# Kernel tuning notes

Hardware: AMD Instinct MI355X
Metric: run time of the kernel (lower is better)

Reference implementation:

```python
import jax, jax.numpy as jnp
import numpy as np

N = 50000      # nodes
E = 1200000    # edges
G = 256        # graphs in batch
H = 64         # hidden_dim
F_IN = 5       # input_dim
L = 3          # num deep GCN layers
EPS_BN = 1e-5
EPS_MSG = 1e-7

def setup_inputs() -> dict:
    key = jax.random.key(0)
    ks = jax.random.split(key, 12)
    r = lambda i, shp, s=0.1: jax.random.normal(ks[i], shp, jnp.float32) * s
    return {
        "x": jax.random.normal(ks[0], (N, F_IN), jnp.float32),
        "edge_index": jax.random.randint(ks[1], (2, E), 0, N),
        "batch_idx": jnp.sort(jax.random.randint(ks[2], (N,), 0, G)),
        "conv1_W": r(3, (F_IN, H)), "conv1_b": jnp.zeros((H,), jnp.float32),
        "bn1_g": jnp.ones((H,), jnp.float32), "bn1_b": jnp.zeros((H,), jnp.float32),
        "ln_g": jnp.ones((L, H), jnp.float32), "ln_b": jnp.zeros((L, H), jnp.float32),
        "prelu_a": jnp.full((L, H), 0.25, jnp.float32),
        "gen_t": jnp.ones((L,), jnp.float32),
        "mlp_W1": r(4, (L, H, 2 * H)), "mlp_b1": jnp.zeros((L, 2 * H), jnp.float32),
        "mlp_bn_g": jnp.ones((L, 2 * H), jnp.float32), "mlp_bn_b": jnp.zeros((L, 2 * H), jnp.float32),
        "mlp_W2": r(5, (L, 2 * H, H)), "mlp_b2": jnp.zeros((L, H), jnp.float32),
        "lin1_W": r(6, ((L + 1) * H * 2, 2 * H)), "lin1_b": jnp.zeros((2 * H,), jnp.float32),
        "lin2_W": r(7, (2 * H, H)), "lin2_b": jnp.zeros((H,), jnp.float32),
        "out_W": r(8, (H, 1)), "out_b": jnp.zeros((1,), jnp.float32),
    }

def _layernorm(x, g, b):
    mu = jnp.mean(x, axis=-1, keepdims=True)
    var = jnp.mean(jnp.square(x - mu), axis=-1, keepdims=True)
    return (x - mu) * jax.lax.rsqrt(var + EPS_BN) * g + b

def _prelu(x, a):
    return jnp.where(x >= 0, x, a * x)

def _bn_eval(x, g, b):
    # eval-mode BatchNorm with running_mean=0, running_var=1
    return x * (g / jnp.sqrt(1.0 + EPS_BN)) + b

def reference(x, edge_index, batch_idx, conv1_W, conv1_b, bn1_g, bn1_b,
              ln_g, ln_b, prelu_a, gen_t, mlp_W1, mlp_b1, mlp_bn_g, mlp_bn_b,
              mlp_W2, mlp_b2, lin1_W, lin1_b, lin2_W, lin2_b, out_W, out_b):
    n = x.shape[0]
    src, dst = edge_index[0], edge_index[1]

    # ---- GCNConv (with self loops, symmetric normalization) ----
    loops = jnp.arange(n)
    row = jnp.concatenate([src, loops])  # [E+N]
    col = jnp.concatenate([dst, loops])
    h = x @ conv1_W
    deg = jax.ops.segment_sum(jnp.ones_like(col, jnp.float32), col, num_segments=n)
    dinv = jnp.where(deg > 0, deg ** -0.5, 0.0)
    norm = dinv[row] * dinv[col]
    h = jax.ops.segment_sum(h[row] * norm[:, None], col, num_segments=n) + conv1_b
    h = _bn_eval(h, bn1_g, bn1_b)
    h = jax.nn.relu(h)

    xs = [h]
    # ---- DeepGCNLayer (res+) x L, GENConv with softmax aggregation ----
    for i in range(ln_g.shape[0]):
        u = _layernorm(h, ln_g[i], ln_b[i])
        u = _prelu(u, prelu_a[i])
        msg = jax.nn.relu(u[src]) + EPS_MSG            # [E, H]
        sc = msg * gen_t[i]
        m = jax.ops.segment_max(sc, dst, num_segments=n)
        e = jnp.exp(sc - m[dst])
        s = jax.ops.segment_sum(e, dst, num_segments=n)
        alpha = e / s[dst]                             # segment-wise softmax per channel
        agg = jax.ops.segment_sum(msg * alpha, dst, num_segments=n) + u  # root add
        z = agg @ mlp_W1[i] + mlp_b1[i]
        z = _bn_eval(z, mlp_bn_g[i], mlp_bn_b[i])
        z = jax.nn.relu(z)
        z = z @ mlp_W2[i] + mlp_b2[i]
        h = h + z                                      # res+
        xs.append(h)

    # ---- JumpingKnowledge cat + global mean/max pool ----
    xc = jnp.concatenate(xs, axis=1)                   # [N, 4H]
    cnt = jax.ops.segment_sum(jnp.ones((n,), jnp.float32), batch_idx, num_segments=G)
    xmean = jax.ops.segment_sum(xc, batch_idx, num_segments=G) / jnp.maximum(cnt, 1.0)[:, None]
    xmax = jax.ops.segment_max(xc, batch_idx, num_segments=G)
    xmax = jnp.where(jnp.isfinite(xmax), xmax, 0.0)
    p = jnp.concatenate([xmean, xmax], axis=1)         # [G, 8H]

    # ---- readout MLP (dropout off in eval) ----
    p = jax.nn.relu(p @ lin1_W + lin1_b)
    p = jax.nn.relu(p @ lin2_W + lin2_b)
    return p @ out_W + out_b
```

## Files before the change

### kernel.cpp

```cpp
#include <hip/hip_runtime.h>
#include <math.h>

#define NND 50000
#define NE  1200000
#define NG  256
#define H   64
#define H2  128
#define H4  256
#define H8  512
#define FIN 5
#define EPS_BN 1e-5f
#define EPS_MSG 1e-7f
#define NB 196
#define TILES 196
#define TCAP 7168
#define EPB 4096
#define NB1 293
#define ELLC 72
#define PC 8
#define MT 64

typedef _Float16 half8 __attribute__((ext_vector_type(8)));
typedef _Float16 half4 __attribute__((ext_vector_type(4)));
typedef float floatx4 __attribute__((ext_vector_type(4)));


__global__ void k_setup(const int* __restrict__ batch, int* tilecur, int* __restrict__ gstart,
                        const float* __restrict__ x, float* __restrict__ xp,
                        const float* __restrict__ W1, const float* __restrict__ W2,
                        _Float16* __restrict__ w1f, _Float16* __restrict__ w2f) {
    int b = blockIdx.x, t = threadIdx.x;
    if (b < NB) {
        int n = b * 256 + t;
        if (n < NND) {
            float a0 = x[n * FIN + 0], a1 = x[n * FIN + 1], a2 = x[n * FIN + 2];
            float a3 = x[n * FIN + 3], a4 = x[n * FIN + 4];
            *(float4*)&xp[n * 8] = make_float4(a0, a1, a2, a3);
            *(float4*)&xp[n * 8 + 4] = make_float4(a4, 0.f, 0.f, 0.f);
        }
        return;
    }
    if (b == NB || b == NB + 1) {
        if (b == NB && t < TILES) tilecur[t] = 0;
        int g = (b - NB) * 256 + t;
        if (g > NG) return;
        int lo = 0, hi = NND;
        while (lo < hi) { int mid = (lo + hi) >> 1; if (batch[mid] < g) lo = mid + 1; else hi = mid; }
        gstart[g] = lo;
        return;
    }
    int tt = (b - NB - 2) * 256 + t;
    if (tt >= 3 * 16 * 64) return;
    int lane = tt & 63, fr = (tt >> 6) & 15, l = tt >> 10;
    {
        int jt = fr >> 1, kf = fr & 1;
        int j = jt * 16 + (lane & 15);
        int k0 = kf * 32 + (lane >> 4) * 8;
#pragma unroll
        for (int i = 0; i < 8; i++)
            w1f[(((size_t)l * 16 + jt * 2 + kf) * 64 + lane) * 8 + i] =
                (_Float16)W1[(size_t)l * H * H2 + (k0 + i) * H2 + j];
    }
    {
        int ct = fr >> 2, k2f = fr & 3;
        int c = ct * 16 + (lane & 15);
        int k0 = k2f * 32 + (lane >> 4) * 8;
#pragma unroll
        for (int i = 0; i < 8; i++)
            w2f[(((size_t)l * 16 + ct * 4 + k2f) * 64 + lane) * 8 + i] =
                (_Float16)W2[(size_t)l * H2 * H + (k0 + i) * H + c];
    }
}


__global__ void __launch_bounds__(256)
k_bin1(const int* __restrict__ ei, int* tilecur, unsigned* __restrict__ tilebuf) {
    __shared__ int cnt[TILES];
    __shared__ int base[TILES];
    int b = blockIdx.x, t = threadIdx.x;
    for (int i = t; i < TILES; i += 256) cnt[i] = 0;
    __syncthreads();
    int e0 = b * EPB;
#pragma unroll
    for (int r = 0; r < EPB / 256; r++) {
        int e = e0 + r * 256 + t;
        if (e < NE) atomicAdd(&cnt[ei[NE + e] >> 8], 1);
    }
    __syncthreads();
    for (int i = t; i < TILES; i += 256) {
        base[i] = atomicAdd(&tilecur[i], cnt[i]);
        cnt[i] = 0;
    }
    __syncthreads();
#pragma unroll
    for (int r = 0; r < EPB / 256; r++) {
        int e = e0 + r * 256 + t;
        if (e < NE) {
            int s = ei[e], d = ei[NE + e];
            int tile = d >> 8;
            int pos = base[tile] + atomicAdd(&cnt[tile], 1);
            if (pos < TCAP)
                tilebuf[(size_t)tile * TCAP + pos] = ((unsigned)s << 8) | (unsigned)(d & 255);
        }
    }
}

__global__ void __launch_bounds__(256)
k_bin2(const int* __restrict__ tilecur, const unsigned* __restrict__ tilebuf,
       unsigned short* __restrict__ ell, int* __restrict__ deg, float* __restrict__ dinv) {
    __shared__ unsigned short ell_l[256 * ELLC];
    __shared__ int cnt[256];
    int tile = blockIdx.x, t = threadIdx.x;
    cnt[t] = 0;
    __syncthreads();
    int n = min(tilecur[tile], TCAP);
    for (int i = t; i < n; i += 256) {
        unsigned v = tilebuf[(size_t)tile * TCAP + i];
        int dl = v & 255u;
        int slot = atomicAdd(&cnt[dl], 1);
        if (slot < ELLC) ell_l[dl * ELLC + slot] = (unsigned short)(v >> 8);
    }
    __syncthreads();
    const unsigned* s32 = (const unsigned*)ell_l;
    unsigned* d32 = (unsigned*)(ell + (size_t)tile * 256 * ELLC);
    for (int i = t; i < 256 * ELLC / 2; i += 256) d32[i] = s32[i];
    int d = tile * 256 + t;
    if (d < NND) {
        deg[d] = min(cnt[t], ELLC);
        dinv[d] = rsqrtf((float)cnt[t] + 1.0f);
    }
}


__global__ void k_gcn(const int* __restrict__ deg, const unsigned short* __restrict__ ell,
                      const float* __restrict__ xp, const float* __restrict__ dinv,
                      const float* __restrict__ W,
                      const float* __restrict__ cb, const float* __restrict__ bg,
                      const float* __restrict__ bb,
                      const float* __restrict__ lg, const float* __restrict__ lb,
                      const float* __restrict__ pa,
                      float* __restrict__ xc, _Float16* __restrict__ u_h) {
    int d = (blockIdx.x * blockDim.x + threadIdx.x) >> 6;
    int lane = threadIdx.x & 63;
    if (d >= NND) return;
    int dg = deg[d];
    size_t base = (size_t)d * ELLC;
    float xw0 = 0.f, xw1 = 0.f, xw2 = 0.f, xw3 = 0.f, xw4 = 0.f;
    for (int i = lane; i < dg; i += 64) {
        int s = (int)ell[base + i];
        float dv = dinv[s];
        float4 a = *(const float4*)&xp[s * 8];
        float a4 = xp[s * 8 + 4];
        xw0 += a.x * dv; xw1 += a.y * dv; xw2 += a.z * dv;
        xw3 += a.w * dv; xw4 += a4 * dv;
    }
#pragma unroll
    for (int off = 1; off <= 32; off <<= 1) {
        xw0 += __shfl_xor(xw0, off, 64);
        xw1 += __shfl_xor(xw1, off, 64);
        xw2 += __shfl_xor(xw2, off, 64);
        xw3 += __shfl_xor(xw3, off, 64);
        xw4 += __shfl_xor(xw4, off, 64);
    }
    float dd = dinv[d];
    float4 xa = *(const float4*)&xp[d * 8];
    float xa4 = xp[d * 8 + 4];
    xw0 += dd * xa.x; xw1 += dd * xa.y; xw2 += dd * xa.z;
    xw3 += dd * xa.w; xw4 += dd * xa4;
    float s_ = xw0 * W[0 * H + lane] + xw1 * W[1 * H + lane] + xw2 * W[2 * H + lane]
             + xw3 * W[3 * H + lane] + xw4 * W[4 * H + lane];
    float v = s_ * dd + cb[lane];
    v = v * (bg[lane] * rsqrtf(1.f + EPS_BN)) + bb[lane];
    float x0 = fmaxf(v, 0.f);
    xc[(size_t)d * H4 + lane] = x0;
    float sum = x0, sq = x0 * x0;
#pragma unroll
    for (int off = 32; off >= 1; off >>= 1) {
        sum += __shfl_xor(sum, off, 64);
        sq  += __shfl_xor(sq,  off, 64);
    }
    float mu  = sum * (1.f / H);
    float var = sq * (1.f / H) - mu * mu;
    float rs = rsqrtf(var + EPS_BN);
    float y = (x0 - mu) * rs * lg[lane] + lb[lane];
    y = (y >= 0.f) ? y : pa[lane] * y;
    u_h[(size_t)d * H + lane] = (_Float16)y;
}


__global__ void k_gen(const int* __restrict__ deg, const unsigned short* __restrict__ ell,
                      const _Float16* __restrict__ u_h,
                      const float* __restrict__ tptr, int li, _Float16* __restrict__ ua_h) {
    int d = (blockIdx.x * blockDim.x + threadIdx.x) >> 6;
    int lane = threadIdx.x & 63;
    if (d >= NND) return;
    int q = lane & 15, eg = lane >> 4;
    float t = tptr[li];
    int dg = deg[d];
    size_t base = (size_t)d * ELLC;
    float4 s4 = {0.f, 0.f, 0.f, 0.f}, n4 = {0.f, 0.f, 0.f, 0.f};
    for (int i0 = 0; i0 < dg; i0 += 64) {
        int idx = i0 + lane;
        int csrv = (idx < dg) ? (int)ell[base + idx] : 0;
        int chunk = min(64, dg - i0);
        for (int j = 0; j < chunk; j += 32) {
            half4 uv[8]; bool ok[8];
#pragma unroll
            for (int b2 = 0; b2 < 8; b2++) {
                int e_rel = j + 4 * b2 + eg;
                int s = __shfl(csrv, e_rel, 64);
                ok[b2] = (e_rel < chunk);
                uv[b2] = (half4){0, 0, 0, 0};
                if (ok[b2]) uv[b2] = *(const half4*)&u_h[(size_t)s * H + 4 * q];
            }
#pragma unroll
            for (int b2 = 0; b2 < 8; b2++) {
                if (ok[b2]) {
                    float m0 = fmaxf((float)uv[b2][0], 0.f) + EPS_MSG;
                    float m1 = fmaxf((float)uv[b2][1], 0.f) + EPS_MSG;
                    float m2 = fmaxf((float)uv[b2][2], 0.f) + EPS_MSG;
                    float m3 = fmaxf((float)uv[b2][3], 0.f) + EPS_MSG;
                    float e0 = __expf(m0 * t - 8.f);
                    float e1 = __expf(m1 * t - 8.f);
                    float e2 = __expf(m2 * t - 8.f);
                    float e3 = __expf(m3 * t - 8.f);
                    s4.x += e0; s4.y += e1; s4.z += e2; s4.w += e3;
                    n4.x += m0 * e0; n4.y += m1 * e1; n4.z += m2 * e2; n4.w += m3 * e3;
                }
            }
        }
    }
#pragma unroll
    for (int off = 16; off <= 32; off <<= 1) {
        s4.x += __shfl_xor(s4.x, off, 64); s4.y += __shfl_xor(s4.y, off, 64);
        s4.z += __shfl_xor(s4.z, off, 64); s4.w += __shfl_xor(s4.w, off, 64);
        n4.x += __shfl_xor(n4.x, off, 64); n4.y += __shfl_xor(n4.y, off, 64);
        n4.z += __shfl_xor(n4.z, off, 64); n4.w += __shfl_xor(n4.w, off, 64);
    }
    if (eg == 0) {
        half4 us = *(const half4*)&u_h[(size_t)d * H + 4 * q];
        float o0 = (float)us[0] + ((s4.x > 0.f) ? n4.x / s4.x : 0.f);
        float o1 = (float)us[1] + ((s4.y > 0.f) ? n4.y / s4.y : 0.f);
        float o2 = (float)us[2] + ((s4.z > 0.f) ? n4.z / s4.z : 0.f);
        float o3 = (float)us[3] + ((s4.w > 0.f) ? n4.w / s4.w : 0.f);
        half4 oh = {(_Float16)o0, (_Float16)o1, (_Float16)o2, (_Float16)o3};
        *(half4*)&ua_h[(size_t)d * H + 4 * q] = oh;
    }
}


__global__ void __launch_bounds__(256)
k_mlp(const _Float16* __restrict__ ua_h,
      const _Float16* __restrict__ w1f, const _Float16* __restrict__ w2f,
      const float* __restrict__ b1,
      const float* __restrict__ bng, const float* __restrict__ bnb,
      const float* __restrict__ b2,
      float* __restrict__ xc, int slice,
      const float* __restrict__ lg, const float* __restrict__ lb,
      const float* __restrict__ pa, _Float16* __restrict__ u_h, int do_ln) {
    __shared__ _Float16 a1[4][2][64][8];
    __shared__ _Float16 a2[4][4][64][8];
    int t = threadIdx.x;
    int w = t >> 6, l = t & 63;
    int nb = blockIdx.x * MT;
    int c_in = l & 15, quad = l >> 4;
    bool wvalid = (nb + 16 * w) < NND;

    {
        int n = t >> 2;
        int k0 = (t & 3) * 16;
        int gn = nb + n;
        half8 h0 = {0,0,0,0,0,0,0,0}, h1 = h0;
        if (gn < NND) {
            h0 = *(const half8*)&ua_h[(size_t)gn * H + k0];
            h1 = *(const half8*)&ua_h[(size_t)gn * H + k0 + 8];
        }
        int mt = n >> 4, kf = k0 >> 5, g0 = (k0 >> 3) & 3;
        *(half8*)&a1[mt][kf][(n & 15) + 16 * g0][0] = h0;
        *(half8*)&a1[mt][kf][(n & 15) + 16 * (g0 + 1)][0] = h1;
    }

    floatx4 acc[8];
#pragma unroll
    for (int jt = 0; jt < 8; jt++) acc[jt] = (floatx4){0.f, 0.f, 0.f, 0.f};
    half8 af0 = *(half8*)&a1[w][0][l][0];
    half8 af1 = *(half8*)&a1[w][1][l][0];
#pragma unroll
    for (int jt = 0; jt < 8; jt++) {
        half8 bf0 = *(const half8*)&w1f[((size_t)(jt * 2 + 0) * 64 + l) * 8];
        half8 bf1 = *(const half8*)&w1f[((size_t)(jt * 2 + 1) * 64 + l) * 8];
        acc[jt] = __builtin_amdgcn_mfma_f32_16x16x32_f16(af0, bf0, acc[jt], 0, 0, 0);
        acc[jt] = __builtin_amdgcn_mfma_f32_16x16x32_f16(af1, bf1, acc[jt], 0, 0, 0);
    }

    {
        float bns = rsqrtf(1.f + EPS_BN);
#pragma unroll
        for (int jt = 0; jt < 8; jt++) {
            int j = jt * 16 + c_in;
            float b1v = b1[j], bsv = bng[j] * bns, bbv = bnb[j];
            int kf2 = jt >> 1;
            int lp = 16 * ((2 * jt + (c_in >> 3)) & 3);
            int ii = c_in & 7;
#pragma unroll
            for (int reg = 0; reg < 4; reg++) {
                float z = fmaxf((acc[jt][reg] + b1v) * bsv + bbv, 0.f);
                a2[w][kf2][quad * 4 + reg + lp][ii] = (_Float16)z;
            }
        }
    }

    floatx4 acc2[4];
#pragma unroll
    for (int ct = 0; ct < 4; ct++) acc2[ct] = (floatx4){0.f, 0.f, 0.f, 0.f};
    half8 a2f[4];
#pragma unroll
    for (int k2f = 0; k2f < 4; k2f++) a2f[k2f] = *(half8*)&a2[w][k2f][l][0];
#pragma unroll
    for (int ct = 0; ct < 4; ct++) {
#pragma unroll
        for (int k2f = 0; k2f < 4; k2f++) {
            half8 bfr = *(const half8*)&w2f[((size_t)(ct * 4 + k2f) * 64 + l) * 8];
            acc2[ct] = __builtin_amdgcn_mfma_f32_16x16x32_f16(a2f[k2f], bfr, acc2[ct], 0, 0, 0);
        }
    }

    float vv[4][4];
#pragma unroll
    for (int ct = 0; ct < 4; ct++) {
        int c = ct * 16 + c_in;
        float b2v = b2[c];
#pragma unroll
        for (int reg = 0; reg < 4; reg++) {
            int node = nb + 16 * w + quad * 4 + reg;
            float v = 0.f;
            if (wvalid) {
                v = xc[(size_t)node * H4 + slice * H + c] + acc2[ct][reg] + b2v;
                xc[(size_t)node * H4 + (slice + 1) * H + c] = v;
            }
            vv[ct][reg] = v;
        }
    }
    if (do_ln) {
#pragma unroll
        for (int reg = 0; reg < 4; reg++) {
            float s = (vv[0][reg] + vv[1][reg]) + (vv[2][reg] + vv[3][reg]);
            float q = (vv[0][reg] * vv[0][reg] + vv[1][reg] * vv[1][reg]) +
                      (vv[2][reg] * vv[2][reg] + vv[3][reg] * vv[3][reg]);
#pragma unroll
            for (int off = 1; off <= 8; off <<= 1) {
                s += __shfl_xor(s, off, 64);
                q += __shfl_xor(q, off, 64);
            }
            float mu = s * (1.f / H);
            float var = q * (1.f / H) - mu * mu;
            float rs = rsqrtf(var + EPS_BN);
            int node = nb + 16 * w + quad * 4 + reg;
#pragma unroll
            for (int ct = 0; ct < 4; ct++) {
                int c = ct * 16 + c_in;
                float y = (vv[ct][reg] - mu) * rs * lg[c] + lb[c];
                y = (y >= 0.f) ? y : pa[c] * y;
                if (wvalid) u_h[(size_t)node * H + c] = (_Float16)y;
            }
        }
    }
}


__global__ void __launch_bounds__(256)
k_pool1(const float* __restrict__ xc, const int* __restrict__ gstart,
        float* __restrict__ psum_p, float* __restrict__ pmax_p) {
    __shared__ float4 ssum[256];
    __shared__ float4 smax[256];
    int b = blockIdx.x;
    int g = b >> 3, k = b & (PC - 1);
    int t = threadIdx.x;
    int start = gstart[g], end = gstart[g + 1];
    int len = end - start;
    int c0 = start + (len * k) / PC;
    int c1 = start + (len * (k + 1)) / PC;
    int q = t & 63, sub = t >> 6;
    float4 sum = {0.f, 0.f, 0.f, 0.f};
    float4 mx = {-INFINITY, -INFINITY, -INFINITY, -INFINITY};
    for (int n = c0 + sub; n < c1; n += 4) {
        float4 v = *(const float4*)&xc[(size_t)n * H4 + 4 * q];
        sum.x += v.x; sum.y += v.y; sum.z += v.z; sum.w += v.w;
        mx.x = fmaxf(mx.x, v.x); mx.y = fmaxf(mx.y, v.y);
        mx.z = fmaxf(mx.z, v.z); mx.w = fmaxf(mx.w, v.w);
    }
    ssum[t] = sum; smax[t] = mx;
    __syncthreads();
    if (t < 64) {
        float4 s0 = ssum[t], s1 = ssum[t + 64], s2 = ssum[t + 128], s3 = ssum[t + 192];
        float4 m0 = smax[t], m1 = smax[t + 64], m2 = smax[t + 128], m3 = smax[t + 192];
        float4 S, M;
        S.x = (s0.x + s1.x) + (s2.x + s3.x);
        S.y = (s0.y + s1.y) + (s2.y + s3.y);
        S.z = (s0.z + s1.z) + (s2.z + s3.z);
        S.w = (s0.w + s1.w) + (s2.w + s3.w);
        M.x = fmaxf(fmaxf(m0.x, m1.x), fmaxf(m2.x, m3.x));
        M.y = fmaxf(fmaxf(m0.y, m1.y), fmaxf(m2.y, m3.y));
        M.z = fmaxf(fmaxf(m0.z, m1.z), fmaxf(m2.z, m3.z));
        M.w = fmaxf(fmaxf(m0.w, m1.w), fmaxf(m2.w, m3.w));
        *(float4*)&psum_p[(size_t)b * H4 + 4 * q] = S;
        *(float4*)&pmax_p[(size_t)b * H4 + 4 * q] = M;
    }
}

__global__ void __launch_bounds__(256)
k_readout(const float* __restrict__ psum_p, const float* __restrict__ pmax_p,
          const int* __restrict__ gstart,
          const float* __restrict__ W1, const float* __restrict__ b1,
          const float* __restrict__ W2, const float* __restrict__ b2,
          const float* __restrict__ Wo, const float* __restrict__ bo,
          float* __restrict__ out) {
    __shared__ float p0_l[H8];
    __shared__ float p1part[2][H2];
    __shared__ float p1_l[H2];
    __shared__ float p2part[4][H];
    __shared__ float p2_l[H];
    int g = blockIdx.x;
    int t = threadIdx.x;

    {
        float s = 0.f, m = -INFINITY;
#pragma unroll
        for (int k = 0; k < PC; k++) {
            s += psum_p[(size_t)(g * PC + k) * H4 + t];
            m = fmaxf(m, pmax_p[(size_t)(g * PC + k) * H4 + t]);
        }
        int cnt = gstart[g + 1] - gstart[g];
        p0_l[t] = s / fmaxf((float)cnt, 1.f);
        p0_l[H4 + t] = (cnt > 0) ? m : 0.f;
    }
    __syncthreads();

    {
        int j = t & 127, h = t >> 7;
        float acc = 0.f;
        int k0 = h * 256;
        for (int k = 0; k < 256; k++) acc += p0_l[k0 + k] * W1[(k0 + k) * H2 + j];
        p1part[h][j] = acc;
    }
    __syncthreads();
    if (t < H2) p1_l[t] = fmaxf(p1part[0][t] + p1part[1][t] + b1[t], 0.f);
    __syncthreads();

    {
        int c = t & 63, h = t >> 6;
        float acc = 0.f;
        int k0 = h * 32;
        for (int k = 0; k < 32; k++) acc += p1_l[k0 + k] * W2[(k0 + k) * H + c];
        p2part[h][c] = acc;
    }
    __syncthreads();
    if (t < H) p2_l[t] = fmaxf(((p2part[0][t] + p2part[1][t]) + (p2part[2][t] + p2part[3][t])) + b2[t], 0.f);
    __syncthreads();

    if (t < 64) {
        float v = p2_l[t] * Wo[t];
#pragma unroll
        for (int off = 32; off >= 1; off >>= 1) v += __shfl_xor(v, off, 64);
        if (t == 0) out[g] = v + bo[0];
    }
}

extern "C" void kernel_launch(void* const* d_in, const int* in_sizes, int n_in,
                              void* d_out, int out_size, void* d_ws, size_t ws_size,
                              hipStream_t stream) {
    const float* x       = (const float*)d_in[0];
    const int*   ei      = (const int*)d_in[1];
    const int*   batch   = (const int*)d_in[2];
    const float* conv1_W = (const float*)d_in[3];
    const float* conv1_b = (const float*)d_in[4];
    const float* bn1_g   = (const float*)d_in[5];
    const float* bn1_b   = (const float*)d_in[6];
    const float* ln_g    = (const float*)d_in[7];
    const float* ln_b    = (const float*)d_in[8];
    const float* prelu_a = (const float*)d_in[9];
    const float* gen_t   = (const float*)d_in[10];
    const float* mlp_W1  = (const float*)d_in[11];
    const float* mlp_b1  = (const float*)d_in[12];
    const float* mlp_bng = (const float*)d_in[13];
    const float* mlp_bnb = (const float*)d_in[14];
    const float* mlp_W2  = (const float*)d_in[15];
    const float* mlp_b2  = (const float*)d_in[16];
    const float* lin1_W  = (const float*)d_in[17];
    const float* lin1_b  = (const float*)d_in[18];
    const float* lin2_W  = (const float*)d_in[19];
    const float* lin2_b  = (const float*)d_in[20];
    const float* out_W   = (const float*)d_in[21];
    const float* out_b   = (const float*)d_in[22];
    float* out = (float*)d_out;

    float* ws   = (float*)d_ws;
    float* xc   = ws;
    float* xp   = xc + (size_t)NND * H4;
    float* dinv = xp + (size_t)NND * 8;
    int* deg    = (int*)(dinv + NND);
    int* gstart = deg + NND;
    int* tilecur = gstart + NG + 1;
    unsigned* tilebuf = (unsigned*)(tilecur + TILES);
    unsigned short* ell = (unsigned short*)(tilebuf + (size_t)TILES * TCAP);
    uintptr_t wb = (uintptr_t)(ell + (size_t)TILES * 256 * ELLC);
    wb = (wb + 15) & ~(uintptr_t)15;
    _Float16* w1f = (_Float16*)wb;
    _Float16* w2f = w1f + 3 * 8192;
    _Float16* u_h  = w2f + 3 * 8192;
    _Float16* ua_h = u_h + (size_t)NND * H;
    uintptr_t pb = (uintptr_t)(ua_h + (size_t)NND * H);
    pb = (pb + 15) & ~(uintptr_t)15;
    float* psum_p = (float*)pb;
    float* pmax_p = psum_p + (size_t)NG * PC * H4;

    const int B = 256;
    const int gNH  = (NND * H) / B;
    const int gMLP = (NND + MT - 1) / MT;

    k_setup<<<NB + 2 + 12, B, 0, stream>>>(batch, tilecur, gstart, x, xp,
                                           mlp_W1, mlp_W2, w1f, w2f);
    k_bin1<<<NB1, B, 0, stream>>>(ei, tilecur, tilebuf);
    k_bin2<<<TILES, B, 0, stream>>>(tilecur, tilebuf, ell, deg, dinv);

    k_gcn<<<gNH, B, 0, stream>>>(deg, ell, xp, dinv, conv1_W, conv1_b, bn1_g, bn1_b,
                                 ln_g, ln_b, prelu_a, xc, u_h);

    for (int i = 0; i < 3; i++) {
        k_gen<<<gNH, B, 0, stream>>>(deg, ell, u_h, gen_t, i, ua_h);
        int do_ln = (i < 2) ? 1 : 0;
        k_mlp<<<gMLP, B, 0, stream>>>(ua_h,
                                      w1f + (size_t)i * 8192, w2f + (size_t)i * 8192,
                                      mlp_b1 + i * H2,
                                      mlp_bng + i * H2, mlp_bnb + i * H2,
                                      mlp_b2 + i * H,
                                      xc, i,
                                      ln_g + (i + 1) * H, ln_b + (i + 1) * H,
                                      prelu_a + (i + 1) * H, u_h, do_ln);
    }

    k_pool1<<<NG * PC, B, 0, stream>>>(xc, gstart, psum_p, pmax_p);
    k_readout<<<NG, B, 0, stream>>>(psum_p, pmax_p, gstart,
                                    lin1_W, lin1_b, lin2_W, lin2_b, out_W, out_b, out);
}
```

Baseline: 339.6 us.

## Store JK concat buffer in fp16 and use 16 lanes per node in GCN

The [N,4H] jumping-knowledge buffer moves from fp32 to fp16 storage, so its writes in the GCN and MLP kernels and its reads in the pool kernel move half the bytes. The GCN kernel now assigns 16 lanes per node, each producing 4 channels, instead of 64 lanes per node. This cuts the grid size and shortens the shuffle reductions. In exchange the residual stream is rounded to fp16 at every layer, which adds accumulated precision error to the pooled outputs.

```diff
diff --git a/kernel.cpp b/kernel.cpp
--- a/kernel.cpp
+++ b/kernel.cpp
@@ -139,14 +139,15 @@
                       const float* __restrict__ bb,
                       const float* __restrict__ lg, const float* __restrict__ lb,
                       const float* __restrict__ pa,
-                      float* __restrict__ xc, _Float16* __restrict__ u_h) {
-    int d = (blockIdx.x * blockDim.x + threadIdx.x) >> 6;
-    int lane = threadIdx.x & 63;
+                      _Float16* __restrict__ xcH, _Float16* __restrict__ u_h) {
+    int tid = blockIdx.x * blockDim.x + threadIdx.x;
+    int d = tid >> 4;
+    int r = threadIdx.x & 15;
     if (d >= NND) return;
     int dg = deg[d];
     size_t base = (size_t)d * ELLC;
     float xw0 = 0.f, xw1 = 0.f, xw2 = 0.f, xw3 = 0.f, xw4 = 0.f;
-    for (int i = lane; i < dg; i += 64) {
+    for (int i = r; i < dg; i += 16) {
         int s = (int)ell[base + i];
         float dv = dinv[s];
         float4 a = *(const float4*)&xp[s * 8];
@@ -155,7 +156,7 @@
         xw3 += a.w * dv; xw4 += a4 * dv;
     }
 #pragma unroll
-    for (int off = 1; off <= 32; off <<= 1) {
+    for (int off = 1; off <= 8; off <<= 1) {
         xw0 += __shfl_xor(xw0, off, 64);
         xw1 += __shfl_xor(xw1, off, 64);
         xw2 += __shfl_xor(xw2, off, 64);
@@ -167,24 +168,41 @@
     float xa4 = xp[d * 8 + 4];
     xw0 += dd * xa.x; xw1 += dd * xa.y; xw2 += dd * xa.z;
     xw3 += dd * xa.w; xw4 += dd * xa4;
-    float s_ = xw0 * W[0 * H + lane] + xw1 * W[1 * H + lane] + xw2 * W[2 * H + lane]
-             + xw3 * W[3 * H + lane] + xw4 * W[4 * H + lane];
-    float v = s_ * dd + cb[lane];
-    v = v * (bg[lane] * rsqrtf(1.f + EPS_BN)) + bb[lane];
-    float x0 = fmaxf(v, 0.f);
-    xc[(size_t)d * H4 + lane] = x0;
-    float sum = x0, sq = x0 * x0;
-#pragma unroll
-    for (int off = 32; off >= 1; off >>= 1) {
+    float bns = rsqrtf(1.f + EPS_BN);
+    float x0[4];
+    float sum = 0.f, sq = 0.f;
+#pragma unroll
+    for (int j = 0; j < 4; j++) {
+        int c = 4 * r + j;
+        float s_ = xw0 * W[c] + xw1 * W[H + c] + xw2 * W[2 * H + c]
+                 + xw3 * W[3 * H + c] + xw4 * W[4 * H + c];
+        float v = s_ * dd + cb[c];
+        v = v * (bg[c] * bns) + bb[c];
+        v = fmaxf(v, 0.f);
+        x0[j] = v;
+        sum += v; sq += v * v;
+    }
+    {
+        half4 xh = {(_Float16)x0[0], (_Float16)x0[1], (_Float16)x0[2], (_Float16)x0[3]};
+        *(half4*)&xcH[(size_t)d * H4 + 4 * r] = xh;
+    }
+#pragma unroll
+    for (int off = 1; off <= 8; off <<= 1) {
         sum += __shfl_xor(sum, off, 64);
         sq  += __shfl_xor(sq,  off, 64);
     }
     float mu  = sum * (1.f / H);
     float var = sq * (1.f / H) - mu * mu;
     float rs = rsqrtf(var + EPS_BN);
-    float y = (x0 - mu) * rs * lg[lane] + lb[lane];
-    y = (y >= 0.f) ? y : pa[lane] * y;
-    u_h[(size_t)d * H + lane] = (_Float16)y;
+    half4 yh;
+#pragma unroll
+    for (int j = 0; j < 4; j++) {
+        int c = 4 * r + j;
+        float y = (x0[j] - mu) * rs * lg[c] + lb[c];
+        y = (y >= 0.f) ? y : pa[c] * y;
+        yh[j] = (_Float16)y;
+    }
+    *(half4*)&u_h[(size_t)d * H + 4 * r] = yh;
 }
 
 
@@ -255,7 +273,7 @@
       const float* __restrict__ b1,
       const float* __restrict__ bng, const float* __restrict__ bnb,
       const float* __restrict__ b2,
-      float* __restrict__ xc, int slice,
+      _Float16* __restrict__ xcH, int slice,
       const float* __restrict__ lg, const float* __restrict__ lb,
       const float* __restrict__ pa, _Float16* __restrict__ u_h, int do_ln) {
     __shared__ _Float16 a1[4][2][64][8];
@@ -335,8 +353,8 @@
             int node = nb + 16 * w + quad * 4 + reg;
             float v = 0.f;
             if (wvalid) {
-                v = xc[(size_t)node * H4 + slice * H + c] + acc2[ct][reg] + b2v;
-                xc[(size_t)node * H4 + (slice + 1) * H + c] = v;
+                v = (float)xcH[(size_t)node * H4 + slice * H + c] + acc2[ct][reg] + b2v;
+                xcH[(size_t)node * H4 + (slice + 1) * H + c] = (_Float16)v;
             }
             vv[ct][reg] = v;
         }
@@ -369,7 +387,7 @@
 
 
 __global__ void __launch_bounds__(256)
-k_pool1(const float* __restrict__ xc, const int* __restrict__ gstart,
+k_pool1(const _Float16* __restrict__ xcH, const int* __restrict__ gstart,
         float* __restrict__ psum_p, float* __restrict__ pmax_p) {
     __shared__ float4 ssum[256];
     __shared__ float4 smax[256];
@@ -384,10 +402,11 @@
     float4 sum = {0.f, 0.f, 0.f, 0.f};
     float4 mx = {-INFINITY, -INFINITY, -INFINITY, -INFINITY};
     for (int n = c0 + sub; n < c1; n += 4) {
-        float4 v = *(const float4*)&xc[(size_t)n * H4 + 4 * q];
-        sum.x += v.x; sum.y += v.y; sum.z += v.z; sum.w += v.w;
-        mx.x = fmaxf(mx.x, v.x); mx.y = fmaxf(mx.y, v.y);
-        mx.z = fmaxf(mx.z, v.z); mx.w = fmaxf(mx.w, v.w);
+        half4 vh = *(const half4*)&xcH[(size_t)n * H4 + 4 * q];
+        float v0 = (float)vh[0], v1 = (float)vh[1], v2 = (float)vh[2], v3 = (float)vh[3];
+        sum.x += v0; sum.y += v1; sum.z += v2; sum.w += v3;
+        mx.x = fmaxf(mx.x, v0); mx.y = fmaxf(mx.y, v1);
+        mx.z = fmaxf(mx.z, v2); mx.w = fmaxf(mx.w, v3);
     }
     ssum[t] = sum; smax[t] = mx;
     __syncthreads();
@@ -495,8 +514,8 @@
     float* out = (float*)d_out;
 
     float* ws   = (float*)d_ws;
-    float* xc   = ws;
-    float* xp   = xc + (size_t)NND * H4;
+    _Float16* xcH = (_Float16*)ws;
+    float* xp   = (float*)(xcH + (size_t)NND * H4);
     float* dinv = xp + (size_t)NND * 8;
     int* deg    = (int*)(dinv + NND);
     int* gstart = deg + NND;
@@ -515,6 +534,7 @@
     float* pmax_p = psum_p + (size_t)NG * PC * H4;
 
     const int B = 256;
+    const int gGCN = (NND * 16 + B - 1) / B;
     const int gNH  = (NND * H) / B;
     const int gMLP = (NND + MT - 1) / MT;
 
@@ -523,8 +543,8 @@
     k_bin1<<<NB1, B, 0, stream>>>(ei, tilecur, tilebuf);
     k_bin2<<<TILES, B, 0, stream>>>(tilecur, tilebuf, ell, deg, dinv);
 
-    k_gcn<<<gNH, B, 0, stream>>>(deg, ell, xp, dinv, conv1_W, conv1_b, bn1_g, bn1_b,
-                                 ln_g, ln_b, prelu_a, xc, u_h);
+    k_gcn<<<gGCN, B, 0, stream>>>(deg, ell, xp, dinv, conv1_W, conv1_b, bn1_g, bn1_b,
+                                  ln_g, ln_b, prelu_a, xcH, u_h);
 
     for (int i = 0; i < 3; i++) {
         k_gen<<<gNH, B, 0, stream>>>(deg, ell, u_h, gen_t, i, ua_h);
@@ -534,12 +554,12 @@
                                       mlp_b1 + i * H2,
                                       mlp_bng + i * H2, mlp_bnb + i * H2,
                                       mlp_b2 + i * H,
-                                      xc, i,
+                                      xcH, i,
                                       ln_g + (i + 1) * H, ln_b + (i + 1) * H,
                                       prelu_a + (i + 1) * H, u_h, do_ln);
     }
 
-    k_pool1<<<NG * PC, B, 0, stream>>>(xc, gstart, psum_p, pmax_p);
+    k_pool1<<<NG * PC, B, 0, stream>>>(xcH, gstart, psum_p, pmax_p);
     k_readout<<<NG, B, 0, stream>>>(psum_p, pmax_p, gstart,
                                     lin1_W, lin1_b, lin2_W, lin2_b, out_W, out_b, out);
 }
```

After: 333.3 us. No clear change (-1.9%).
